# Optimization experiments

Measured on AMD Instinct MI355X. Metric: run time of the kernel, lower is better.

The kernel has to match this reference:

```python
import jax, jax.numpy as jnp
import numpy as np

D_MODEL = 1024
NUM_HEADS = 16
DEPTH = D_MODEL // NUM_HEADS


def setup_inputs() -> dict:
    key = jax.random.key(0)
    ks = jax.random.split(key, 9)
    B, S = 2, 2048
    s = 1.0 / np.sqrt(D_MODEL)
    inp = {
        "inputs": jax.random.normal(ks[0], (B, S, D_MODEL), dtype=jnp.float32),
        "wq": jax.random.normal(ks[1], (D_MODEL, D_MODEL), dtype=jnp.float32) * s,
        "bq": jnp.zeros((D_MODEL,), dtype=jnp.float32),
        "wk": jax.random.normal(ks[2], (D_MODEL, D_MODEL), dtype=jnp.float32) * s,
        "bk": jnp.zeros((D_MODEL,), dtype=jnp.float32),
        "wv": jax.random.normal(ks[3], (D_MODEL, D_MODEL), dtype=jnp.float32) * s,
        "bv": jnp.zeros((D_MODEL,), dtype=jnp.float32),
        "wo": jax.random.normal(ks[4], (D_MODEL, D_MODEL), dtype=jnp.float32) * s,
        "bo": jnp.zeros((D_MODEL,), dtype=jnp.float32),
    }
    return inp


def _split_heads(x, B):
    # [B, S, D] -> [B, H, S, depth]
    S = x.shape[1]
    return x.reshape(B, S, NUM_HEADS, DEPTH).transpose(0, 2, 1, 3)


def reference(inputs, wq, bq, wk, bk, wv, bv, wo, bo):
    B, S, _ = inputs.shape
    q = _split_heads(inputs @ wq + bq, B)  # [B,H,S,d]
    k = _split_heads(inputs @ wk + bk, B)
    v = _split_heads(inputs @ wv + bv, B)
    scale = 1.0 / jnp.sqrt(jnp.asarray(DEPTH, dtype=inputs.dtype))
    logits = jnp.einsum("bhqd,bhkd->bhqk", q, k) * scale  # [B,H,S,S]
    attn = jax.nn.softmax(logits, axis=-1)
    out = jnp.einsum("bhqk,bhkd->bhqd", attn, v)  # [B,H,S,d]
    out = out.transpose(0, 2, 1, 3).reshape(B, S, D_MODEL)
    return out @ wo + bo
```

## Files before the change

kernel.cpp:

```cpp
#include <hip/hip_runtime.h>
#include <math.h>

#define SEQ     2048
#define DM      1024
#define NH      16
#define DEPTH   64
#define MTOT    4096

typedef __attribute__((ext_vector_type(8))) __bf16 bf16x8;
typedef __attribute__((ext_vector_type(4))) float  f32x4;
typedef __attribute__((ext_vector_type(4))) short  short4v;

static __device__ inline short f2bf(float f) {
    union { float f; unsigned u; } v; v.f = f;
    unsigned r = v.u + 0x7FFFu + ((v.u >> 16) & 1u);
    return (short)(r >> 16);
}
static __device__ inline unsigned bfbits_fast(float f) {
    union { float f; unsigned u; } v; v.f = f;
    return (v.u + 0x8000u) >> 16;
}

#define GLOBAL_AS(p) ((const __attribute__((address_space(1))) void*)(p))
#define LDS_AS(p)    ((__attribute__((address_space(3))) void*)(p))

#define K2  0.18033688011112043f
#define C2 -17.31234049066756f
#define EXP2(x) __builtin_amdgcn_exp2f(x)

__global__ __launch_bounds__(256)
void prep(const float* __restrict__ X,
          const float* __restrict__ w0, const float* __restrict__ w1,
          const float* __restrict__ w2, const float* __restrict__ w3,
          short* __restrict__ Xb,
          short* __restrict__ o0, short* __restrict__ o1,
          short* __restrict__ o2, short* __restrict__ o3) {
    const int t = threadIdx.x;
    const int z = blockIdx.z;
    if (z >= 4) {
        int r0 = (z - 4) * 1024 + blockIdx.x * 64;
        int c0 = blockIdx.y * 64;
        #pragma unroll
        for (int i = 0; i < 4; i++) {
            int row = r0 + i * 16 + (t >> 4);
            int c4  = c0 + (t & 15) * 4;
            float4 v = *(const float4*)&X[(size_t)row * DM + c4];
            short4v o; o.x = f2bf(v.x); o.y = f2bf(v.y); o.z = f2bf(v.z); o.w = f2bf(v.w);
            *(short4v*)&Xb[(size_t)row * DM + c4] = o;
        }
        return;
    }
    const float* W; short* O;
    switch (z) {
        case 0: W = w0; O = o0; break;
        case 1: W = w1; O = o1; break;
        case 2: W = w2; O = o2; break;
        default: W = w3; O = o3; break;
    }
    __shared__ float Tf[64][65];
    const int k0 = blockIdx.x * 64, n0 = blockIdx.y * 64;
    #pragma unroll
    for (int i = 0; i < 4; i++) {
        int row = i * 16 + (t >> 4);
        int c4  = (t & 15) * 4;
        float4 v = *(const float4*)&W[(size_t)(k0 + row) * DM + n0 + c4];
        Tf[row][c4 + 0] = v.x; Tf[row][c4 + 1] = v.y;
        Tf[row][c4 + 2] = v.z; Tf[row][c4 + 3] = v.w;
    }
    __syncthreads();
    #pragma unroll
    for (int i = 0; i < 4; i++) {
        int nrow = i * 16 + (t >> 4);
        int kc4  = (t & 15) * 4;
        short4v o;
        o.x = f2bf(Tf[kc4 + 0][nrow]); o.y = f2bf(Tf[kc4 + 1][nrow]);
        o.z = f2bf(Tf[kc4 + 2][nrow]); o.w = f2bf(Tf[kc4 + 3][nrow]);
        *(short4v*)&O[(size_t)(n0 + nrow) * DM + k0 + kc4] = o;
    }
}

__global__ __launch_bounds__(256)
void gemm_qkv(const short* __restrict__ Xb,
              const short* __restrict__ Wqt, const short* __restrict__ Wkt,
              const short* __restrict__ Wvt,
              const float* __restrict__ bq, const float* __restrict__ bk,
              const float* __restrict__ bv,
              short* __restrict__ Qw, short* __restrict__ Kw,
              short* __restrict__ Vtw) {
    const int z = blockIdx.z;
    const short* A; const short* B; const float* bias;
    if (z == 0)      { A = Xb;  B = Wqt; bias = bq; }
    else if (z == 1) { A = Xb;  B = Wkt; bias = bk; }
    else             { A = Wvt; B = Xb;  bias = bv; }
    const int bx = blockIdx.x;
    int m0, n0;
    if (z < 2) { n0 = (bx & 7) * 128; m0 = (bx >> 3) * 128; }
    else       { m0 = (bx & 7) * 128; n0 = (bx >> 3) * 128; }

    __shared__ short As[128 * 32];
    __shared__ short Bs[128 * 32];
    const int t = threadIdx.x, lane = t & 63, w = t >> 6;
    const int lx = lane & 15, quad = lane >> 4;
    const int wm = (w & 1) * 64, wn = (w >> 1) * 64;
    const int r = lane >> 2, c8 = (lane & 3) * 8;

    f32x4 acc[4][4];
    #pragma unroll
    for (int i = 0; i < 4; i++)
        #pragma unroll
        for (int j = 0; j < 4; j++)
            acc[i][j] = (f32x4){0.f, 0.f, 0.f, 0.f};

    for (int k0 = 0; k0 < DM; k0 += 32) {
        #pragma unroll
        for (int j = 0; j < 2; j++) {
            int rb = (w * 2 + j) * 16;
            __builtin_amdgcn_global_load_lds(
                GLOBAL_AS(A + (size_t)(m0 + rb + r) * DM + k0 + c8),
                LDS_AS(As + rb * 32), 16, 0, 0);
            __builtin_amdgcn_global_load_lds(
                GLOBAL_AS(B + (size_t)(n0 + rb + r) * DM + k0 + c8),
                LDS_AS(Bs + rb * 32), 16, 0, 0);
        }
        __syncthreads();

        bf16x8 af[4], bfr[4];
        #pragma unroll
        for (int mt = 0; mt < 4; mt++)
            af[mt] = *(bf16x8*)&As[(wm + mt * 16 + lx) * 32 + quad * 8];
        #pragma unroll
        for (int nt = 0; nt < 4; nt++)
            bfr[nt] = *(bf16x8*)&Bs[(wn + nt * 16 + lx) * 32 + quad * 8];
        #pragma unroll
        for (int mt = 0; mt < 4; mt++)
            #pragma unroll
            for (int nt = 0; nt < 4; nt++)
                acc[mt][nt] = __builtin_amdgcn_mfma_f32_16x16x32_bf16(
                    af[mt], bfr[nt], acc[mt][nt], 0, 0, 0);
        __syncthreads();
    }

    #pragma unroll
    for (int mt = 0; mt < 4; mt++) {
        #pragma unroll
        for (int nt = 0; nt < 4; nt++) {
            #pragma unroll
            for (int reg = 0; reg < 4; reg++) {
                int row = m0 + wm + mt * 16 + quad * 4 + reg;
                int col = n0 + wn + nt * 16 + lx;
                if (z == 0) {
                    Qw[(size_t)row * DM + col] = f2bf(acc[mt][nt][reg] + bias[col]);
                } else if (z == 1) {
                    Kw[(size_t)row * DM + col] = f2bf(acc[mt][nt][reg] + bias[col]);
                } else {
                    int scol  = col & 2047;
                    int kbase = scol & ~63;
                    int c     = ((nt >> 1) * 32) + ((scol & 15) * 2) + (nt & 1);
                    Vtw[(size_t)(col >> 11) * ((size_t)NH * DEPTH * SEQ)
                        + (size_t)row * SEQ + kbase + c]
                        = f2bf(acc[mt][nt][reg] + bias[row]);
                }
            }
        }
    }
}

__global__ __launch_bounds__(256)
void gemm_out(const short* __restrict__ A, const short* __restrict__ B,
              const float* __restrict__ bias, float* __restrict__ C) {
    __shared__ short As[128 * 32];
    __shared__ short Bs[64 * 32];
    const int t = threadIdx.x, lane = t & 63, w = t >> 6;
    const int lx = lane & 15, quad = lane >> 4;
    const int n0 = blockIdx.x * 64, m0 = blockIdx.y * 128;
    const int wm = (w & 1) * 64, wn = (w >> 1) * 32;
    const int r = lane >> 2, c8 = (lane & 3) * 8;

    f32x4 acc[4][2];
    #pragma unroll
    for (int i = 0; i < 4; i++)
        #pragma unroll
        for (int j = 0; j < 2; j++)
            acc[i][j] = (f32x4){0.f, 0.f, 0.f, 0.f};

    for (int k0 = 0; k0 < DM; k0 += 32) {
        #pragma unroll
        for (int j = 0; j < 2; j++) {
            int rb = w * 32 + j * 16;
            __builtin_amdgcn_global_load_lds(
                GLOBAL_AS(A + (size_t)(m0 + rb + r) * DM + k0 + c8),
                LDS_AS(As + rb * 32), 16, 0, 0);
        }
        {
            int rb = w * 16;
            __builtin_amdgcn_global_load_lds(
                GLOBAL_AS(B + (size_t)(n0 + rb + r) * DM + k0 + c8),
                LDS_AS(Bs + rb * 32), 16, 0, 0);
        }
        __syncthreads();

        bf16x8 af[4], bfr[2];
        #pragma unroll
        for (int mt = 0; mt < 4; mt++)
            af[mt] = *(bf16x8*)&As[(wm + mt * 16 + lx) * 32 + quad * 8];
        #pragma unroll
        for (int nt = 0; nt < 2; nt++)
            bfr[nt] = *(bf16x8*)&Bs[(wn + nt * 16 + lx) * 32 + quad * 8];
        #pragma unroll
        for (int mt = 0; mt < 4; mt++)
            #pragma unroll
            for (int nt = 0; nt < 2; nt++)
                acc[mt][nt] = __builtin_amdgcn_mfma_f32_16x16x32_bf16(
                    af[mt], bfr[nt], acc[mt][nt], 0, 0, 0);
        __syncthreads();
    }

    #pragma unroll
    for (int mt = 0; mt < 4; mt++)
        #pragma unroll
        for (int nt = 0; nt < 2; nt++)
            #pragma unroll
            for (int reg = 0; reg < 4; reg++) {
                int row = m0 + wm + mt * 16 + quad * 4 + reg;
                int col = n0 + wn + nt * 16 + lx;
                C[(size_t)row * DM + col] = acc[mt][nt][reg] + bias[col];
            }
}

__global__ __launch_bounds__(256)
void flash_mfma(const short* __restrict__ Q, const short* __restrict__ K,
                const short* __restrict__ Vt, short* __restrict__ O) {
    __shared__ short Ks[2][64 * 32];
    __shared__ short Vs[2][64 * 32];
    __shared__ short Ps[128 * 72];

    const int t = threadIdx.x, lane = t & 63, w = t >> 6;
    const int lx = lane & 15, quad = lane >> 4;
    const int h = blockIdx.y, bb = blockIdx.z;
    const int q0 = blockIdx.x * 128;
    const int r = lane >> 2, c8 = (lane & 3) * 8;

    bf16x8 qa[2][2];
    #pragma unroll
    for (int mt = 0; mt < 2; mt++)
        #pragma unroll
        for (int ks = 0; ks < 2; ks++)
            qa[mt][ks] = *(const bf16x8*)&Q[(size_t)(bb * SEQ + q0 + w * 32 + mt * 16 + lx) * DM
                                            + h * DEPTH + ks * 32 + quad * 8];

    f32x4 of[2][4];
    float l_acc[2][4];
    #pragma unroll
    for (int mt = 0; mt < 2; mt++) {
        #pragma unroll
        for (int dt = 0; dt < 4; dt++) of[mt][dt] = (f32x4){0.f, 0.f, 0.f, 0.f};
        #pragma unroll
        for (int reg = 0; reg < 4; reg++) l_acc[mt][reg] = 0.f;
    }

    const short* Kb = K  + (size_t)bb * SEQ * DM + h * DEPTH;
    const short* Vb = Vt + (size_t)(bb * NH + h) * DEPTH * SEQ;

    for (int kt = 0; kt < SEQ / 64; kt++) {
        __syncthreads();
        const int kbase = kt * 64;
        {
            const short* kg = Kb + (size_t)(kbase + w * 16 + r) * DM;
            __builtin_amdgcn_global_load_lds(GLOBAL_AS(kg + c8),      LDS_AS(&Ks[0][w * 16 * 32]), 16, 0, 0);
            __builtin_amdgcn_global_load_lds(GLOBAL_AS(kg + 32 + c8), LDS_AS(&Ks[1][w * 16 * 32]), 16, 0, 0);
            const short* vg = Vb + (size_t)(w * 16 + r) * SEQ + kbase;
            __builtin_amdgcn_global_load_lds(GLOBAL_AS(vg + c8),      LDS_AS(&Vs[0][w * 16 * 32]), 16, 0, 0);
            __builtin_amdgcn_global_load_lds(GLOBAL_AS(vg + 32 + c8), LDS_AS(&Vs[1][w * 16 * 32]), 16, 0, 0);
        }
        __syncthreads();

        f32x4 s[2][4];
        #pragma unroll
        for (int mt = 0; mt < 2; mt++)
            #pragma unroll
            for (int nt = 0; nt < 4; nt++)
                s[mt][nt] = (f32x4){0.f, 0.f, 0.f, 0.f};
        #pragma unroll
        for (int ks = 0; ks < 2; ks++) {
            bf16x8 kb[4];
            #pragma unroll
            for (int nt = 0; nt < 4; nt++)
                kb[nt] = *(bf16x8*)&Ks[ks][(nt * 16 + lx) * 32 + quad * 8];
            #pragma unroll
            for (int mt = 0; mt < 2; mt++)
                #pragma unroll
                for (int nt = 0; nt < 4; nt++)
                    s[mt][nt] = __builtin_amdgcn_mfma_f32_16x16x32_bf16(
                        qa[mt][ks], kb[nt], s[mt][nt], 0, 0, 0);
        }

        #pragma unroll
        for (int mt = 0; mt < 2; mt++) {
            #pragma unroll
            for (int reg = 0; reg < 4; reg++) {
                float p0 = EXP2(fmaf(s[mt][0][reg], K2, C2));
                float p1 = EXP2(fmaf(s[mt][1][reg], K2, C2));
                float p2 = EXP2(fmaf(s[mt][2][reg], K2, C2));
                float p3 = EXP2(fmaf(s[mt][3][reg], K2, C2));
                l_acc[mt][reg] += (p0 + p1) + (p2 + p3);
                int rowoff = (w * 32 + mt * 16 + quad * 4 + reg) * 72;
                unsigned pk01 = bfbits_fast(p0) | (bfbits_fast(p1) << 16);
                unsigned pk23 = bfbits_fast(p2) | (bfbits_fast(p3) << 16);
                *(unsigned*)&Ps[rowoff + 2 * lx]      = pk01;
                *(unsigned*)&Ps[rowoff + 32 + 2 * lx] = pk23;
            }
        }

        #pragma unroll
        for (int ks = 0; ks < 2; ks++) {
            bf16x8 vb[4], pa[2];
            #pragma unroll
            for (int dt = 0; dt < 4; dt++)
                vb[dt] = *(bf16x8*)&Vs[ks][(dt * 16 + lx) * 32 + quad * 8];
            #pragma unroll
            for (int mt = 0; mt < 2; mt++)
                pa[mt] = *(bf16x8*)&Ps[(w * 32 + mt * 16 + lx) * 72 + ks * 32 + quad * 8];
            #pragma unroll
            for (int mt = 0; mt < 2; mt++)
                #pragma unroll
                for (int dt = 0; dt < 4; dt++)
                    of[mt][dt] = __builtin_amdgcn_mfma_f32_16x16x32_bf16(
                        pa[mt], vb[dt], of[mt][dt], 0, 0, 0);
        }
    }

    #pragma unroll
    for (int mt = 0; mt < 2; mt++) {
        #pragma unroll
        for (int reg = 0; reg < 4; reg++) {
            float l = l_acc[mt][reg];
            l += __shfl_xor(l, 1);
            l += __shfl_xor(l, 2);
            l += __shfl_xor(l, 4);
            l += __shfl_xor(l, 8);
            float inv = 1.0f / l;
            size_t row = (size_t)bb * SEQ + q0 + w * 32 + mt * 16 + quad * 4 + reg;
            #pragma unroll
            for (int dt = 0; dt < 4; dt++)
                O[row * DM + h * DEPTH + dt * 16 + lx] = f2bf(of[mt][dt][reg] * inv);
        }
    }
}

extern "C" void kernel_launch(void* const* d_in, const int* in_sizes, int n_in,
                              void* d_out, int out_size, void* d_ws, size_t ws_size,
                              hipStream_t stream) {
    const float* X  = (const float*)d_in[0];
    const float* wq = (const float*)d_in[1];
    const float* bq = (const float*)d_in[2];
    const float* wk = (const float*)d_in[3];
    const float* bk = (const float*)d_in[4];
    const float* wv = (const float*)d_in[5];
    const float* bv = (const float*)d_in[6];
    const float* wo = (const float*)d_in[7];
    const float* bo = (const float*)d_in[8];
    float* out = (float*)d_out;

    short* Xb  = (short*)d_ws;
    short* Wqt = Xb  + (size_t)MTOT * DM;
    short* Wkt = Wqt + (size_t)DM * DM;
    short* Wvt = Wkt + (size_t)DM * DM;
    short* Wot = Wvt + (size_t)DM * DM;
    short* Qw  = Wot + (size_t)DM * DM;
    short* Kw  = Qw  + (size_t)MTOT * DM;
    short* Vtw = Kw  + (size_t)MTOT * DM;
    short* AO  = Vtw + (size_t)MTOT * DM;

    hipLaunchKernelGGL(prep, dim3(16, 16, 8), dim3(256), 0, stream,
                       X, wq, wk, wv, wo, Xb, Wqt, Wkt, Wvt, Wot);

    hipLaunchKernelGGL(gemm_qkv, dim3(256, 1, 3), dim3(256), 0, stream,
                       Xb, Wqt, Wkt, Wvt, bq, bk, bv, Qw, Kw, Vtw);

    hipLaunchKernelGGL(flash_mfma, dim3(SEQ / 128, NH, 2), dim3(256), 0, stream,
                       Qw, Kw, Vtw, AO);

    hipLaunchKernelGGL(gemm_out, dim3(16, 32), dim3(256), 0, stream,
                       AO, Wot, bo, out);
}
```

Baseline: 207.1 us.

## XOR-swizzle LDS tiles to avoid bank conflicts and vectorize V-transpose stores

The global-to-LDS DMA loads now permute the source column chunk by an XOR of row bits, and the fragment reads apply the matching XOR. Reads of 16-row MFMA fragments then spread across LDS banks instead of colliding, in the QKV GEMM, the output GEMM and the flash-attention K/V tiles. The V-transpose epilogue also packs two bf16 values into 32-bit stores with a hoisted base address, replacing scattered 16-bit stores. The risk is swizzle-index mistakes that would silently corrupt the operands.

```diff
diff --git a/kernel.cpp b/kernel.cpp
--- a/kernel.cpp
+++ b/kernel.cpp
@@ -16,6 +16,10 @@
     unsigned r = v.u + 0x7FFFu + ((v.u >> 16) & 1u);
     return (short)(r >> 16);
 }
+static __device__ inline unsigned bfbits(float f) {
+    union { float f; unsigned u; } v; v.f = f;
+    return (v.u + 0x7FFFu + ((v.u >> 16) & 1u)) >> 16;
+}
 static __device__ inline unsigned bfbits_fast(float f) {
     union { float f; unsigned u; } v; v.f = f;
     return (v.u + 0x8000u) >> 16;
@@ -27,6 +31,9 @@
 #define K2  0.18033688011112043f
 #define C2 -17.31234049066756f
 #define EXP2(x) __builtin_amdgcn_exp2f(x)
+
+#define DMA_SRC_C8(lane)  ((((lane) & 3) ^ (((lane) >> 3) & 3)) * 8)
+#define FRAG_C8(lx,quad)  ((((quad) ^ (((lx) >> 1) & 3))) * 8)
 
 __global__ __launch_bounds__(256)
 void prep(const float* __restrict__ X,
@@ -102,7 +109,8 @@
     const int t = threadIdx.x, lane = t & 63, w = t >> 6;
     const int lx = lane & 15, quad = lane >> 4;
     const int wm = (w & 1) * 64, wn = (w >> 1) * 64;
-    const int r = lane >> 2, c8 = (lane & 3) * 8;
+    const int r = lane >> 2;
+    const int cs8 = DMA_SRC_C8(lane);
 
     f32x4 acc[4][4];
     #pragma unroll
@@ -110,16 +118,18 @@
         #pragma unroll
         for (int j = 0; j < 4; j++)
             acc[i][j] = (f32x4){0.f, 0.f, 0.f, 0.f};
+
+    const int fa = FRAG_C8(lx, quad);
 
     for (int k0 = 0; k0 < DM; k0 += 32) {
         #pragma unroll
         for (int j = 0; j < 2; j++) {
             int rb = (w * 2 + j) * 16;
             __builtin_amdgcn_global_load_lds(
-                GLOBAL_AS(A + (size_t)(m0 + rb + r) * DM + k0 + c8),
+                GLOBAL_AS(A + (size_t)(m0 + rb + r) * DM + k0 + cs8),
                 LDS_AS(As + rb * 32), 16, 0, 0);
             __builtin_amdgcn_global_load_lds(
-                GLOBAL_AS(B + (size_t)(n0 + rb + r) * DM + k0 + c8),
+                GLOBAL_AS(B + (size_t)(n0 + rb + r) * DM + k0 + cs8),
                 LDS_AS(Bs + rb * 32), 16, 0, 0);
         }
         __syncthreads();
@@ -127,10 +137,10 @@
         bf16x8 af[4], bfr[4];
         #pragma unroll
         for (int mt = 0; mt < 4; mt++)
-            af[mt] = *(bf16x8*)&As[(wm + mt * 16 + lx) * 32 + quad * 8];
+            af[mt] = *(bf16x8*)&As[(wm + mt * 16 + lx) * 32 + fa];
         #pragma unroll
         for (int nt = 0; nt < 4; nt++)
-            bfr[nt] = *(bf16x8*)&Bs[(wn + nt * 16 + lx) * 32 + quad * 8];
+            bfr[nt] = *(bf16x8*)&Bs[(wn + nt * 16 + lx) * 32 + fa];
         #pragma unroll
         for (int mt = 0; mt < 4; mt++)
             #pragma unroll
@@ -140,26 +150,35 @@
         __syncthreads();
     }
 
-    #pragma unroll
-    for (int mt = 0; mt < 4; mt++) {
-        #pragma unroll
-        for (int nt = 0; nt < 4; nt++) {
+    if (z < 2) {
+        short* Cp = (z == 0) ? Qw : Kw;
+        #pragma unroll
+        for (int mt = 0; mt < 4; mt++)
+            #pragma unroll
+            for (int nt = 0; nt < 4; nt++)
+                #pragma unroll
+                for (int reg = 0; reg < 4; reg++) {
+                    int row = m0 + wm + mt * 16 + quad * 4 + reg;
+                    int col = n0 + wn + nt * 16 + lx;
+                    Cp[(size_t)row * DM + col] = f2bf(acc[mt][nt][reg] + bias[col]);
+                }
+    } else {
+        int colbase = n0 + wn;
+        int bsel    = colbase >> 11;
+        int scolb   = colbase & 2047;
+        int kb      = scolb & ~63;
+        short* Vbh  = Vtw + (size_t)bsel * ((size_t)NH * DEPTH * SEQ);
+        #pragma unroll
+        for (int mt = 0; mt < 4; mt++) {
             #pragma unroll
             for (int reg = 0; reg < 4; reg++) {
                 int row = m0 + wm + mt * 16 + quad * 4 + reg;
-                int col = n0 + wn + nt * 16 + lx;
-                if (z == 0) {
-                    Qw[(size_t)row * DM + col] = f2bf(acc[mt][nt][reg] + bias[col]);
-                } else if (z == 1) {
-                    Kw[(size_t)row * DM + col] = f2bf(acc[mt][nt][reg] + bias[col]);
-                } else {
-                    int scol  = col & 2047;
-                    int kbase = scol & ~63;
-                    int c     = ((nt >> 1) * 32) + ((scol & 15) * 2) + (nt & 1);
-                    Vtw[(size_t)(col >> 11) * ((size_t)NH * DEPTH * SEQ)
-                        + (size_t)row * SEQ + kbase + c]
-                        = f2bf(acc[mt][nt][reg] + bias[row]);
-                }
+                float bb = bias[row];
+                unsigned lo = bfbits(acc[mt][0][reg] + bb) | (bfbits(acc[mt][1][reg] + bb) << 16);
+                unsigned hi = bfbits(acc[mt][2][reg] + bb) | (bfbits(acc[mt][3][reg] + bb) << 16);
+                size_t base = (size_t)row * SEQ + kb + 2 * lx;
+                *(unsigned*)&Vbh[base]      = lo;
+                *(unsigned*)&Vbh[base + 32] = hi;
             }
         }
     }
@@ -174,7 +193,9 @@
     const int lx = lane & 15, quad = lane >> 4;
     const int n0 = blockIdx.x * 64, m0 = blockIdx.y * 128;
     const int wm = (w & 1) * 64, wn = (w >> 1) * 32;
-    const int r = lane >> 2, c8 = (lane & 3) * 8;
+    const int r = lane >> 2;
+    const int cs8 = DMA_SRC_C8(lane);
+    const int fa  = FRAG_C8(lx, quad);
 
     f32x4 acc[4][2];
     #pragma unroll
@@ -188,13 +209,13 @@
         for (int j = 0; j < 2; j++) {
             int rb = w * 32 + j * 16;
             __builtin_amdgcn_global_load_lds(
-                GLOBAL_AS(A + (size_t)(m0 + rb + r) * DM + k0 + c8),
+                GLOBAL_AS(A + (size_t)(m0 + rb + r) * DM + k0 + cs8),
                 LDS_AS(As + rb * 32), 16, 0, 0);
         }
         {
             int rb = w * 16;
             __builtin_amdgcn_global_load_lds(
-                GLOBAL_AS(B + (size_t)(n0 + rb + r) * DM + k0 + c8),
+                GLOBAL_AS(B + (size_t)(n0 + rb + r) * DM + k0 + cs8),
                 LDS_AS(Bs + rb * 32), 16, 0, 0);
         }
         __syncthreads();
@@ -202,10 +223,10 @@
         bf16x8 af[4], bfr[2];
         #pragma unroll
         for (int mt = 0; mt < 4; mt++)
-            af[mt] = *(bf16x8*)&As[(wm + mt * 16 + lx) * 32 + quad * 8];
+            af[mt] = *(bf16x8*)&As[(wm + mt * 16 + lx) * 32 + fa];
         #pragma unroll
         for (int nt = 0; nt < 2; nt++)
-            bfr[nt] = *(bf16x8*)&Bs[(wn + nt * 16 + lx) * 32 + quad * 8];
+            bfr[nt] = *(bf16x8*)&Bs[(wn + nt * 16 + lx) * 32 + fa];
         #pragma unroll
         for (int mt = 0; mt < 4; mt++)
             #pragma unroll
@@ -238,7 +259,9 @@
     const int lx = lane & 15, quad = lane >> 4;
     const int h = blockIdx.y, bb = blockIdx.z;
     const int q0 = blockIdx.x * 128;
-    const int r = lane >> 2, c8 = (lane & 3) * 8;
+    const int r = lane >> 2;
+    const int cs8 = DMA_SRC_C8(lane);
+    const int fa  = FRAG_C8(lx, quad);
 
     bf16x8 qa[2][2];
     #pragma unroll
@@ -266,11 +289,11 @@
         const int kbase = kt * 64;
         {
             const short* kg = Kb + (size_t)(kbase + w * 16 + r) * DM;
-            __builtin_amdgcn_global_load_lds(GLOBAL_AS(kg + c8),      LDS_AS(&Ks[0][w * 16 * 32]), 16, 0, 0);
-            __builtin_amdgcn_global_load_lds(GLOBAL_AS(kg + 32 + c8), LDS_AS(&Ks[1][w * 16 * 32]), 16, 0, 0);
+            __builtin_amdgcn_global_load_lds(GLOBAL_AS(kg + cs8),      LDS_AS(&Ks[0][w * 16 * 32]), 16, 0, 0);
+            __builtin_amdgcn_global_load_lds(GLOBAL_AS(kg + 32 + cs8), LDS_AS(&Ks[1][w * 16 * 32]), 16, 0, 0);
             const short* vg = Vb + (size_t)(w * 16 + r) * SEQ + kbase;
-            __builtin_amdgcn_global_load_lds(GLOBAL_AS(vg + c8),      LDS_AS(&Vs[0][w * 16 * 32]), 16, 0, 0);
-            __builtin_amdgcn_global_load_lds(GLOBAL_AS(vg + 32 + c8), LDS_AS(&Vs[1][w * 16 * 32]), 16, 0, 0);
+            __builtin_amdgcn_global_load_lds(GLOBAL_AS(vg + cs8),      LDS_AS(&Vs[0][w * 16 * 32]), 16, 0, 0);
+            __builtin_amdgcn_global_load_lds(GLOBAL_AS(vg + 32 + cs8), LDS_AS(&Vs[1][w * 16 * 32]), 16, 0, 0);
         }
         __syncthreads();
 
@@ -285,7 +308,7 @@
             bf16x8 kb[4];
             #pragma unroll
             for (int nt = 0; nt < 4; nt++)
-                kb[nt] = *(bf16x8*)&Ks[ks][(nt * 16 + lx) * 32 + quad * 8];
+                kb[nt] = *(bf16x8*)&Ks[ks][(nt * 16 + lx) * 32 + fa];
             #pragma unroll
             for (int mt = 0; mt < 2; mt++)
                 #pragma unroll
@@ -316,7 +339,7 @@
             bf16x8 vb[4], pa[2];
             #pragma unroll
             for (int dt = 0; dt < 4; dt++)
-                vb[dt] = *(bf16x8*)&Vs[ks][(dt * 16 + lx) * 32 + quad * 8];
+                vb[dt] = *(bf16x8*)&Vs[ks][(dt * 16 + lx) * 32 + fa];
             #pragma unroll
             for (int mt = 0; mt < 2; mt++)
                 pa[mt] = *(bf16x8*)&Ps[(w * 32 + mt * 16 + lx) * 72 + ks * 32 + quad * 8];
```

Result: no change. 211.3 us (+2.0%).
